# Optimization experiments

Hardware: AMD Instinct MI355X
Metric: run time of the kernel (lower is better)

## Reference

```python
import jax, jax.numpy as jnp
import numpy as np

B, S, D = 4, 2048, 512
H, DK, DV = 8, 64, 64
DFF = 2048
LN_EPS = 1e-5


def _layernorm(x, g, b):
    mu = jnp.mean(x, axis=-1, keepdims=True)
    var = jnp.mean(jnp.square(x - mu), axis=-1, keepdims=True)
    return (x - mu) * jax.lax.rsqrt(var + LN_EPS) * g + b


def setup_inputs() -> dict:
    key = jax.random.key(0)
    ks = jax.random.split(key, 9)
    def xavier(k, shape):
        fan_out, fan_in = shape
        std = np.sqrt(2.0 / (fan_in + fan_out))
        return jax.random.normal(k, shape, jnp.float32) * std
    GELU_GAIN = 1.85
    return {
        "x": jax.random.normal(ks[0], (B, S, D), jnp.float32),
        "attention_mask": jax.random.randint(ks[1], (B, S), 0, 2).astype(bool),
        "Wq": xavier(ks[2], (H * DK, D)),
        "Wk": xavier(ks[3], (H * DK, D)),
        "Wv": xavier(ks[4], (H * DV, D)),
        "Wp": xavier(ks[5], (D, H * DV)),
        "W1": xavier(ks[6], (DFF, D)) * GELU_GAIN,
        "b1": jnp.zeros((DFF,), jnp.float32),
        "W2": xavier(ks[7], (D, DFF)),
        "b2": jnp.zeros((D,), jnp.float32),
        "ln1_g": jnp.ones((D,), jnp.float32),
        "ln1_b": jnp.zeros((D,), jnp.float32),
        "ln2_g": jnp.ones((D,), jnp.float32),
        "ln2_b": jnp.zeros((D,), jnp.float32),
    }


def reference(x, attention_mask, Wq, Wk, Wv, Wp, W1, b1, W2, b2,
              ln1_g, ln1_b, ln2_g, ln2_b):
    b, s, d = x.shape
    residual = x
    q = (x @ Wq.T).reshape(b, s, H, DK)  # [B,S,H,DK]
    k = (x @ Wk.T).reshape(b, s, H, DK)
    v = (x @ Wv.T).reshape(b, s, H, DV)
    score = jnp.einsum("bshd,bthd->bhst", q, k) * (DK ** -0.5)  # [B,H,S,S]
    # subtractive mask: score -= 100 * not(mask)
    score = score - 100.0 * (~attention_mask)[:, None, None, :].astype(score.dtype)
    p = jax.nn.softmax(score, axis=-1)
    ctx = jnp.einsum("bhst,bthd->bshd", p, v).reshape(b, s, H * DV)
    att = ctx @ Wp.T  # dropout p=0.1 is identity in eval
    h = _layernorm(att + residual, ln1_g, ln1_b)
    ff = jax.nn.gelu(h @ W1.T + b1, approximate=False) @ W2.T + b2
    out = _layernorm(ff + h, ln2_g, ln2_b)
    return out
```

## Files before the change

### kernel.cpp

```cpp
#include <hip/hip_runtime.h>
#include <cstdint>
#include <cstddef>

#define B_ 4
#define S_ 2048
#define D_ 512
#define H_ 8
#define DK_ 64
#define DFF_ 2048

using s16x8  = __attribute__((ext_vector_type(8))) short;
using bf16x8 = __attribute__((ext_vector_type(8))) __bf16;
using f32x4  = __attribute__((ext_vector_type(4))) float;

__device__ __forceinline__ short f2bf(float f) {
  unsigned u = __builtin_bit_cast(unsigned, f);
  u += 0x7FFFu + ((u >> 16) & 1u);
  return (short)(u >> 16);
}
__device__ __forceinline__ float bf2f(short s) {
  unsigned u = ((unsigned)(unsigned short)s) << 16;
  return __builtin_bit_cast(float, u);
}

__device__ __forceinline__ void gl2lds16(const void* g, void* l) {
  __builtin_amdgcn_global_load_lds(
      (const __attribute__((address_space(1))) void*)g,
      (__attribute__((address_space(3))) void*)l, 16, 0, 0);
}

__global__ __launch_bounds__(256)
void cvt_all(const float* __restrict__ x, const float* __restrict__ Wq,
             const float* __restrict__ Wk, const float* __restrict__ Wv,
             const float* __restrict__ Wp, const float* __restrict__ W1,
             const float* __restrict__ W2,
             short* __restrict__ xb, short* __restrict__ wqkv,
             short* __restrict__ wp, short* __restrict__ w1, short* __restrict__ w2) {
  int blk = blockIdx.x;
  const float* src; short* dst; int off;
  if (blk < 4096)      { src = x;  dst = xb;            off = blk; }
  else if (blk < 4352) { src = Wq; dst = wqkv;          off = blk - 4096; }
  else if (blk < 4608) { src = Wk; dst = wqkv + 262144; off = blk - 4352; }
  else if (blk < 4864) { src = Wv; dst = wqkv + 524288; off = blk - 4608; }
  else if (blk < 5120) { src = Wp; dst = wp;            off = blk - 4864; }
  else if (blk < 6144) { src = W1; dst = w1;            off = blk - 5120; }
  else                 { src = W2; dst = w2;            off = blk - 6144; }
  int i = (off * 256 + threadIdx.x) * 4;
  float4 v = *(const float4*)(src + i);
  *(short4*)(dst + i) = make_short4(f2bf(v.x), f2bf(v.y), f2bf(v.z), f2bf(v.w));
}

__global__ __launch_bounds__(256)
void mask_all(const void* __restrict__ m, float* __restrict__ mb) {
  __shared__ unsigned red[4];
  const unsigned* mw = (const unsigned*)m;
  const int t = threadIdx.x;
  unsigned v = 0;
#pragma unroll
  for (int i = 0; i < 8; ++i) v |= mw[t + i * 256];
#pragma unroll
  for (int s = 1; s < 64; s <<= 1) v |= __shfl_xor(v, s);
  if ((t & 63) == 0) red[t >> 6] = v;
  __syncthreads();
  unsigned f = red[0] | red[1] | red[2] | red[3];
  int i = blockIdx.x * 256 + t;
  int val;
  if ((f & ~1u) == 0u)            val = ((const int*)m)[i];
  else if (f == 0x3F800000u)      val = (((const float*)m)[i] != 0.0f);
  else                            val = ((const unsigned char*)m)[i];
  mb[i] = val ? 0.0f : -100.0f;
}

template <int MODE>
__global__ __launch_bounds__(256)
void gemm_bt(const short* __restrict__ A, const short* __restrict__ B,
             int M, int N, int K,
             const float* __restrict__ aux1,
             void* __restrict__ out0, void* __restrict__ out1, void* __restrict__ out2) {
  __shared__ alignas(16) short As[128][64];
  __shared__ alignas(16) short Bs[128][64];

  const int tid  = threadIdx.x;
  const int lane = tid & 63;
  const int wave = tid >> 6;
  const int quad = lane >> 4;
  const int l16  = lane & 15;
  const int wm   = (wave >> 1) * 64;
  const int wn   = (wave & 1) * 64;
  const int bm   = blockIdx.x * 128;
  const int bn   = blockIdx.y * 128;
  const int Kh   = K / gridDim.z;
  const int koff = blockIdx.z * Kh;

  const int srow8 = lane >> 3;
  const int pb    = lane & 7;

  f32x4 acc[4][4] = {};

  for (int k0 = 0; k0 < Kh; k0 += 64) {
#pragma unroll
    for (int i = 0; i < 4; ++i) {
      const int rr = wave * 32 + i * 8 + srow8;
      const int cb = pb ^ (rr & 7);
      gl2lds16(A + (size_t)(bm + rr) * K + koff + k0 + cb * 8, &As[wave * 32 + i * 8][0]);
      gl2lds16(B + (size_t)(bn + rr) * K + koff + k0 + cb * 8, &Bs[wave * 32 + i * 8][0]);
    }
    __syncthreads();

#pragma unroll
    for (int c = 0; c < 2; ++c) {
      bf16x8 a[4], b[4];
#pragma unroll
      for (int i = 0; i < 4; ++i) {
        const int row = wm + i * 16 + l16;
        const int pba = (c * 4 + quad) ^ (row & 7);
        a[i] = __builtin_bit_cast(bf16x8, *(const s16x8*)&As[row][pba * 8]);
      }
#pragma unroll
      for (int j = 0; j < 4; ++j) {
        const int row = wn + j * 16 + l16;
        const int pbb = (c * 4 + quad) ^ (row & 7);
        b[j] = __builtin_bit_cast(bf16x8, *(const s16x8*)&Bs[row][pbb * 8]);
      }
#pragma unroll
      for (int i = 0; i < 4; ++i)
#pragma unroll
        for (int j = 0; j < 4; ++j)
          acc[i][j] = __builtin_amdgcn_mfma_f32_16x16x32_bf16(a[i], b[j], acc[i][j], 0, 0, 0);
    }
    __syncthreads();
  }

#pragma unroll
  for (int i = 0; i < 4; ++i) {
    const int m0 = bm + wm + i * 16 + quad * 4;
#pragma unroll
    for (int j = 0; j < 4; ++j) {
      const int n = bn + wn + j * 16 + l16;
      if constexpr (MODE == 0) {
        const int bb = m0 >> 11, ss0 = m0 & 2047;
        if (n < 512) {
          short4 pk = make_short4(f2bf(acc[i][j][0] * 0.125f), f2bf(acc[i][j][1] * 0.125f),
                                  f2bf(acc[i][j][2] * 0.125f), f2bf(acc[i][j][3] * 0.125f));
          *(short4*)((short*)out0 +
              ((((size_t)bb * H_ + (n >> 6)) * 64 + (n & 63)) * S_ + ss0)) = pk;
        } else if (n >= 1024) {
          const int nn = n - 1024;
          short4 pk = make_short4(f2bf(acc[i][j][0]), f2bf(acc[i][j][1]),
                                  f2bf(acc[i][j][2]), f2bf(acc[i][j][3]));
          *(short4*)((short*)out2 +
              ((((size_t)bb * H_ + (nn >> 6)) * 64 + (nn & 63)) * S_ + ss0)) = pk;
        } else {
          const int nn = n - 512;
          const size_t rowb = ((size_t)bb * H_ + (nn >> 6)) * S_ + ss0;
#pragma unroll
          for (int rr = 0; rr < 4; ++rr)
            ((short*)out1)[(rowb + rr) * 64 + (nn & 63)] = f2bf(acc[i][j][rr]);
        }
      } else if constexpr (MODE == 1) {
        float* dst = (float*)out0 + (size_t)blockIdx.z * M * N;
#pragma unroll
        for (int rr = 0; rr < 4; ++rr)
          dst[(size_t)(m0 + rr) * N + n] = acc[i][j][rr];
      } else {
#pragma unroll
        for (int rr = 0; rr < 4; ++rr) {
          float t = acc[i][j][rr] + aux1[n];
          float gl = 0.5f * t * (1.0f + erff(t * 0.70710678118f));
          ((short*)out0)[(size_t)(m0 + rr) * N + n] = f2bf(gl);
        }
      }
    }
  }
}

__global__ __launch_bounds__(256)
void flash_attn_mfma(const short* __restrict__ QTg, const short* __restrict__ Kb,
                     const short* __restrict__ Vtg, const float* __restrict__ maskbias,
                     short* __restrict__ ctxb) {
  __shared__ alignas(16) short Ks[64][72];
  __shared__ alignas(16) short Vt[64][72];
  __shared__ alignas(16) short Ps[4][32][72];
  __shared__ alignas(16) float mrow[S_];

  const int b = blockIdx.z, h = blockIdx.y;
  const int tid = threadIdx.x;
  const int w = tid >> 6, lane = tid & 63;
  const int quad = lane >> 4, l16 = lane & 15;
  const size_t base  = ((size_t)(b * H_ + h)) * S_ * DK_;
  const size_t baseT = ((size_t)(b * H_ + h)) * DK_ * S_;
  const int q0 = blockIdx.x * 128;

  {
    const float4* mp = (const float4*)(maskbias + (size_t)b * S_);
    ((float4*)mrow)[tid]       = mp[tid];
    ((float4*)mrow)[tid + 256] = mp[tid + 256];
  }

  bf16x8 qa[2][2];
#pragma unroll
  for (int st = 0; st < 2; ++st) {
    const int q = q0 + w * 32 + st * 16 + l16;
#pragma unroll
    for (int c = 0; c < 2; ++c) {
      s16x8 t;
#pragma unroll
      for (int j = 0; j < 8; ++j)
        t[j] = QTg[baseT + (size_t)(c * 32 + quad * 8 + j) * S_ + q];
      qa[st][c] = __builtin_bit_cast(bf16x8, t);
    }
  }

  f32x4 Oc[2][4] = {};
  float li[2][4] = {};

  const int r = tid >> 2, c16 = (tid & 3) * 16;
  const short* kp = Kb  + base  + (size_t)r * 64 + c16;
  const short* vp = Vtg + baseT + (size_t)r * S_ + c16;

  s16x8 kr0 = *(const s16x8*)(kp);
  s16x8 kr1 = *(const s16x8*)(kp + 8);
  s16x8 vr0 = *(const s16x8*)(vp);
  s16x8 vr1 = *(const s16x8*)(vp + 8);

  for (int t0 = 0; t0 < S_; t0 += 64) {
    __syncthreads();
    *(s16x8*)&Ks[r][c16]     = kr0;
    *(s16x8*)&Ks[r][c16 + 8] = kr1;
    *(s16x8*)&Vt[r][c16]     = vr0;
    *(s16x8*)&Vt[r][c16 + 8] = vr1;
    __syncthreads();

    if (t0 + 64 < S_) {
      kr0 = *(const s16x8*)(kp + (size_t)(t0 + 64) * 64);
      kr1 = *(const s16x8*)(kp + (size_t)(t0 + 64) * 64 + 8);
      vr0 = *(const s16x8*)(vp + t0 + 64);
      vr1 = *(const s16x8*)(vp + t0 + 64 + 8);
    }

    f32x4 sc[2][4] = {};
#pragma unroll
    for (int c = 0; c < 2; ++c) {
#pragma unroll
      for (int jt = 0; jt < 4; ++jt) {
        bf16x8 kb = __builtin_bit_cast(bf16x8,
            *(const s16x8*)&Ks[jt * 16 + l16][c * 32 + quad * 8]);
        sc[0][jt] = __builtin_amdgcn_mfma_f32_16x16x32_bf16(qa[0][c], kb, sc[0][jt], 0, 0, 0);
        sc[1][jt] = __builtin_amdgcn_mfma_f32_16x16x32_bf16(qa[1][c], kb, sc[1][jt], 0, 0, 0);
      }
    }

    float mb4[4];
#pragma unroll
    for (int jt = 0; jt < 4; ++jt) mb4[jt] = mrow[t0 + jt * 16 + l16];
#pragma unroll
    for (int st = 0; st < 2; ++st) {
#pragma unroll
      for (int jt = 0; jt < 4; ++jt) {
#pragma unroll
        for (int rr = 0; rr < 4; ++rr) {
          float p = __expf(sc[st][jt][rr] + mb4[jt]);
          unsigned u = __builtin_bit_cast(unsigned, p) & 0xFFFF0000u;
          li[st][rr] += __builtin_bit_cast(float, u);
          Ps[w][st * 16 + quad * 4 + rr][jt * 16 + l16] = (short)(u >> 16);
        }
      }
    }

#pragma unroll
    for (int c = 0; c < 2; ++c) {
      bf16x8 pa0 = __builtin_bit_cast(bf16x8,
          *(const s16x8*)&Ps[w][l16][c * 32 + quad * 8]);
      bf16x8 pa1 = __builtin_bit_cast(bf16x8,
          *(const s16x8*)&Ps[w][16 + l16][c * 32 + quad * 8]);
#pragma unroll
      for (int dt = 0; dt < 4; ++dt) {
        bf16x8 vb = __builtin_bit_cast(bf16x8,
            *(const s16x8*)&Vt[dt * 16 + l16][c * 32 + quad * 8]);
        Oc[0][dt] = __builtin_amdgcn_mfma_f32_16x16x32_bf16(pa0, vb, Oc[0][dt], 0, 0, 0);
        Oc[1][dt] = __builtin_amdgcn_mfma_f32_16x16x32_bf16(pa1, vb, Oc[1][dt], 0, 0, 0);
      }
    }
  }

#pragma unroll
  for (int st = 0; st < 2; ++st) {
#pragma unroll
    for (int rr = 0; rr < 4; ++rr) {
      float l = li[st][rr];
#pragma unroll
      for (int m = 1; m < 16; m <<= 1) l += __shfl_xor(l, m);
      float inv = 1.f / l;
      const size_t row = (size_t)b * S_ + q0 + w * 32 + st * 16 + quad * 4 + rr;
#pragma unroll
      for (int dt = 0; dt < 4; ++dt)
        ctxb[row * (H_ * DK_) + h * 64 + dt * 16 + l16] = f2bf(Oc[st][dt][rr] * inv);
    }
  }
}

__global__ __launch_bounds__(256)
void ln_fused(const float* __restrict__ p0, const float* __restrict__ p1,
              const float* __restrict__ xres, const short* __restrict__ hres,
              const float* __restrict__ bias,
              const float* __restrict__ g, const float* __restrict__ bb,
              float* __restrict__ out32, short* __restrict__ outb) {
  const int wave = threadIdx.x >> 6, lane = threadIdx.x & 63;
  const int token = blockIdx.x * 4 + wave;
  const size_t off = (size_t)token * D_;
  const int c = lane * 8;

  float v[8];
  {
    float4 a0 = *(const float4*)(p0 + off + c);
    float4 a1 = *(const float4*)(p0 + off + c + 4);
    float4 b0 = *(const float4*)(p1 + off + c);
    float4 b1 = *(const float4*)(p1 + off + c + 4);
    v[0]=a0.x+b0.x; v[1]=a0.y+b0.y; v[2]=a0.z+b0.z; v[3]=a0.w+b0.w;
    v[4]=a1.x+b1.x; v[5]=a1.y+b1.y; v[6]=a1.z+b1.z; v[7]=a1.w+b1.w;
  }
  if (xres) {
    float4 x0 = *(const float4*)(xres + off + c);
    float4 x1 = *(const float4*)(xres + off + c + 4);
    v[0]+=x0.x; v[1]+=x0.y; v[2]+=x0.z; v[3]+=x0.w;
    v[4]+=x1.x; v[5]+=x1.y; v[6]+=x1.z; v[7]+=x1.w;
  }
  if (hres) {
    short4 h0 = *(const short4*)(hres + off + c);
    short4 h1 = *(const short4*)(hres + off + c + 4);
    v[0]+=bf2f(h0.x); v[1]+=bf2f(h0.y); v[2]+=bf2f(h0.z); v[3]+=bf2f(h0.w);
    v[4]+=bf2f(h1.x); v[5]+=bf2f(h1.y); v[6]+=bf2f(h1.z); v[7]+=bf2f(h1.w);
  }
  if (bias) {
    float4 c0 = *(const float4*)(bias + c);
    float4 c1 = *(const float4*)(bias + c + 4);
    v[0]+=c0.x; v[1]+=c0.y; v[2]+=c0.z; v[3]+=c0.w;
    v[4]+=c1.x; v[5]+=c1.y; v[6]+=c1.z; v[7]+=c1.w;
  }

  float sum = 0.f;
#pragma unroll
  for (int i = 0; i < 8; ++i) sum += v[i];
#pragma unroll
  for (int m = 1; m < 64; m <<= 1) sum += __shfl_xor(sum, m);
  float mu = sum * (1.0f / D_);
  float vs = 0.f;
#pragma unroll
  for (int i = 0; i < 8; ++i) { v[i] -= mu; vs += v[i] * v[i]; }
#pragma unroll
  for (int m = 1; m < 64; m <<= 1) vs += __shfl_xor(vs, m);
  float rstd = rsqrtf(vs * (1.0f / D_) + 1e-5f);
#pragma unroll
  for (int i = 0; i < 8; ++i) {
    float val = v[i] * rstd * g[c + i] + bb[c + i];
    if (out32) out32[off + c + i] = val;
    if (outb)  outb[off + c + i] = f2bf(val);
  }
}

constexpr size_t OFF_XB   = 0;
constexpr size_t OFF_WQKV = 8388608;
constexpr size_t OFF_WP   = 9961472;
constexpr size_t OFF_W1   = 10485760;
constexpr size_t OFF_W2   = 12582912;
constexpr size_t OFF_QT   = 14680064;
constexpr size_t OFF_K    = 23068672;
constexpr size_t OFF_VT   = 31457280;
constexpr size_t OFF_CTX  = 39845888;
constexpr size_t OFF_P0   = 48234496;
constexpr size_t OFF_P1   = 65011712;
constexpr size_t OFF_HB   = 81788928;
constexpr size_t OFF_FF1  = 14680064;
constexpr size_t OFF_MB   = 90177536;
constexpr size_t WS_NEED  = 90210304;

extern "C" void kernel_launch(void* const* d_in, const int* in_sizes, int n_in,
                              void* d_out, int out_size, void* d_ws, size_t ws_size,
                              hipStream_t stream) {
  if (ws_size < WS_NEED) return;

  const float* x    = (const float*)d_in[0];
  const void*  msk  = d_in[1];
  const float* Wq   = (const float*)d_in[2];
  const float* Wk   = (const float*)d_in[3];
  const float* Wv   = (const float*)d_in[4];
  const float* Wp   = (const float*)d_in[5];
  const float* W1   = (const float*)d_in[6];
  const float* b1   = (const float*)d_in[7];
  const float* W2   = (const float*)d_in[8];
  const float* b2   = (const float*)d_in[9];
  const float* ln1g = (const float*)d_in[10];
  const float* ln1b = (const float*)d_in[11];
  const float* ln2g = (const float*)d_in[12];
  const float* ln2b = (const float*)d_in[13];

  char* ws = (char*)d_ws;
  short* xb    = (short*)(ws + OFF_XB);
  short* wqkv  = (short*)(ws + OFF_WQKV);
  short* Wpb   = (short*)(ws + OFF_WP);
  short* W1b   = (short*)(ws + OFF_W1);
  short* W2b   = (short*)(ws + OFF_W2);
  short* QTb   = (short*)(ws + OFF_QT);
  short* Kbh   = (short*)(ws + OFF_K);
  short* VTb   = (short*)(ws + OFF_VT);
  short* ctxb  = (short*)(ws + OFF_CTX);
  float* p0    = (float*)(ws + OFF_P0);
  short* hb    = (short*)(ws + OFF_HB);
  short* ff1b  = (short*)(ws + OFF_FF1);
  float* mbias = (float*)(ws + OFF_MB);

  mask_all<<<32, 256, 0, stream>>>(msk, mbias);

  cvt_all<<<7168, 256, 0, stream>>>(x, Wq, Wk, Wv, Wp, W1, W2,
                                    xb, wqkv, Wpb, W1b, W2b);

  gemm_bt<0><<<dim3(64, 12, 1), 256, 0, stream>>>(xb, wqkv, 8192, 1536, 512,
                                                  nullptr, QTb, Kbh, VTb);

  flash_attn_mfma<<<dim3(S_ / 128, H_, B_), 256, 0, stream>>>(QTb, Kbh, VTb, mbias, ctxb);

  gemm_bt<1><<<dim3(64, 4, 2), 256, 0, stream>>>(ctxb, Wpb, 8192, 512, 512,
                                                 nullptr, p0, nullptr, nullptr);

  ln_fused<<<2048, 256, 0, stream>>>(p0, p0 + (size_t)8192 * 512, x, nullptr, nullptr,
                                     ln1g, ln1b, nullptr, hb);

  gemm_bt<2><<<dim3(64, 16, 1), 256, 0, stream>>>(hb, W1b, 8192, 2048, 512,
                                                  b1, ff1b, nullptr, nullptr);

  gemm_bt<1><<<dim3(64, 4, 2), 256, 0, stream>>>(ff1b, W2b, 8192, 512, 2048,
                                                 nullptr, p0, nullptr, nullptr);

  ln_fused<<<2048, 256, 0, stream>>>(p0, p0 + (size_t)8192 * 512, nullptr, hb, b2,
                                     ln2g, ln2b, (float*)d_out, nullptr);
}
```

Before: 325.0 us.

## Load K/V MFMA fragments directly from global memory, swizzle P tile in LDS

```diff
diff --git a/kernel.cpp b/kernel.cpp
--- a/kernel.cpp
+++ b/kernel.cpp
@@ -174,12 +174,10 @@
   }
 }
 
-__global__ __launch_bounds__(256)
+__global__ __launch_bounds__(256, 2)
 void flash_attn_mfma(const short* __restrict__ QTg, const short* __restrict__ Kb,
                      const short* __restrict__ Vtg, const float* __restrict__ maskbias,
                      short* __restrict__ ctxb) {
-  __shared__ alignas(16) short Ks[64][72];
-  __shared__ alignas(16) short Vt[64][72];
   __shared__ alignas(16) short Ps[4][32][72];
   __shared__ alignas(16) float mrow[S_];
 
@@ -196,6 +194,7 @@
     ((float4*)mrow)[tid]       = mp[tid];
     ((float4*)mrow)[tid + 256] = mp[tid + 256];
   }
+  __syncthreads();
 
   bf16x8 qa[2][2];
 #pragma unroll
@@ -213,38 +212,18 @@
 
   f32x4 Oc[2][4] = {};
   float li[2][4] = {};
-
-  const int r = tid >> 2, c16 = (tid & 3) * 16;
-  const short* kp = Kb  + base  + (size_t)r * 64 + c16;
-  const short* vp = Vtg + baseT + (size_t)r * S_ + c16;
-
-  s16x8 kr0 = *(const s16x8*)(kp);
-  s16x8 kr1 = *(const s16x8*)(kp + 8);
-  s16x8 vr0 = *(const s16x8*)(vp);
-  s16x8 vr1 = *(const s16x8*)(vp + 8);
+  const int swz = l16 & 7;
+  const short* kfrag = Kb  + base  + quad * 8;
+  const short* vfrag = Vtg + baseT + quad * 8;
 
   for (int t0 = 0; t0 < S_; t0 += 64) {
-    __syncthreads();
-    *(s16x8*)&Ks[r][c16]     = kr0;
-    *(s16x8*)&Ks[r][c16 + 8] = kr1;
-    *(s16x8*)&Vt[r][c16]     = vr0;
-    *(s16x8*)&Vt[r][c16 + 8] = vr1;
-    __syncthreads();
-
-    if (t0 + 64 < S_) {
-      kr0 = *(const s16x8*)(kp + (size_t)(t0 + 64) * 64);
-      kr1 = *(const s16x8*)(kp + (size_t)(t0 + 64) * 64 + 8);
-      vr0 = *(const s16x8*)(vp + t0 + 64);
-      vr1 = *(const s16x8*)(vp + t0 + 64 + 8);
-    }
-
     f32x4 sc[2][4] = {};
 #pragma unroll
     for (int c = 0; c < 2; ++c) {
 #pragma unroll
       for (int jt = 0; jt < 4; ++jt) {
         bf16x8 kb = __builtin_bit_cast(bf16x8,
-            *(const s16x8*)&Ks[jt * 16 + l16][c * 32 + quad * 8]);
+            *(const s16x8*)(kfrag + (size_t)(t0 + jt * 16 + l16) * 64 + c * 32));
         sc[0][jt] = __builtin_amdgcn_mfma_f32_16x16x32_bf16(qa[0][c], kb, sc[0][jt], 0, 0, 0);
         sc[1][jt] = __builtin_amdgcn_mfma_f32_16x16x32_bf16(qa[1][c], kb, sc[1][jt], 0, 0, 0);
       }
@@ -262,7 +241,9 @@
           float p = __expf(sc[st][jt][rr] + mb4[jt]);
           unsigned u = __builtin_bit_cast(unsigned, p) & 0xFFFF0000u;
           li[st][rr] += __builtin_bit_cast(float, u);
-          Ps[w][st * 16 + quad * 4 + rr][jt * 16 + l16] = (short)(u >> 16);
+          const int row = st * 16 + quad * 4 + rr;
+          const int blk = (jt * 2 + (l16 >> 3)) ^ (row & 7);
+          Ps[w][row][blk * 8 + (l16 & 7)] = (short)(u >> 16);
         }
       }
     }
@@ -270,13 +251,13 @@
 #pragma unroll
     for (int c = 0; c < 2; ++c) {
       bf16x8 pa0 = __builtin_bit_cast(bf16x8,
-          *(const s16x8*)&Ps[w][l16][c * 32 + quad * 8]);
+          *(const s16x8*)&Ps[w][l16][(((c * 4 + quad) ^ swz)) * 8]);
       bf16x8 pa1 = __builtin_bit_cast(bf16x8,
-          *(const s16x8*)&Ps[w][16 + l16][c * 32 + quad * 8]);
+          *(const s16x8*)&Ps[w][16 + l16][(((c * 4 + quad) ^ swz)) * 8]);
 #pragma unroll
       for (int dt = 0; dt < 4; ++dt) {
         bf16x8 vb = __builtin_bit_cast(bf16x8,
-            *(const s16x8*)&Vt[dt * 16 + l16][c * 32 + quad * 8]);
+            *(const s16x8*)(vfrag + (size_t)(dt * 16 + l16) * S_ + t0 + c * 32));
         Oc[0][dt] = __builtin_amdgcn_mfma_f32_16x16x32_bf16(pa0, vb, Oc[0][dt], 0, 0, 0);
         Oc[1][dt] = __builtin_amdgcn_mfma_f32_16x16x32_bf16(pa1, vb, Oc[1][dt], 0, 0, 0);
       }
```

Measured after the change: 405.0 us. 24.6% more time.

## Fuse mask preprocessing into attention kernel and swizzle P tile in LDS

Applied to the files above, without the earlier changes.

```diff
diff --git a/kernel.cpp b/kernel.cpp
--- a/kernel.cpp
+++ b/kernel.cpp
@@ -50,27 +50,6 @@
   *(short4*)(dst + i) = make_short4(f2bf(v.x), f2bf(v.y), f2bf(v.z), f2bf(v.w));
 }
 
-__global__ __launch_bounds__(256)
-void mask_all(const void* __restrict__ m, float* __restrict__ mb) {
-  __shared__ unsigned red[4];
-  const unsigned* mw = (const unsigned*)m;
-  const int t = threadIdx.x;
-  unsigned v = 0;
-#pragma unroll
-  for (int i = 0; i < 8; ++i) v |= mw[t + i * 256];
-#pragma unroll
-  for (int s = 1; s < 64; s <<= 1) v |= __shfl_xor(v, s);
-  if ((t & 63) == 0) red[t >> 6] = v;
-  __syncthreads();
-  unsigned f = red[0] | red[1] | red[2] | red[3];
-  int i = blockIdx.x * 256 + t;
-  int val;
-  if ((f & ~1u) == 0u)            val = ((const int*)m)[i];
-  else if (f == 0x3F800000u)      val = (((const float*)m)[i] != 0.0f);
-  else                            val = ((const unsigned char*)m)[i];
-  mb[i] = val ? 0.0f : -100.0f;
-}
-
 template <int MODE>
 __global__ __launch_bounds__(256)
 void gemm_bt(const short* __restrict__ A, const short* __restrict__ B,
@@ -176,12 +155,13 @@
 
 __global__ __launch_bounds__(256)
 void flash_attn_mfma(const short* __restrict__ QTg, const short* __restrict__ Kb,
-                     const short* __restrict__ Vtg, const float* __restrict__ maskbias,
+                     const short* __restrict__ Vtg, const void* __restrict__ mraw,
                      short* __restrict__ ctxb) {
   __shared__ alignas(16) short Ks[64][72];
   __shared__ alignas(16) short Vt[64][72];
-  __shared__ alignas(16) short Ps[4][32][72];
+  __shared__ alignas(16) short Ps[4][32][64];
   __shared__ alignas(16) float mrow[S_];
+  __shared__ unsigned red[4];
 
   const int b = blockIdx.z, h = blockIdx.y;
   const int tid = threadIdx.x;
@@ -192,9 +172,25 @@
   const int q0 = blockIdx.x * 128;
 
   {
-    const float4* mp = (const float4*)(maskbias + (size_t)b * S_);
-    ((float4*)mrow)[tid]       = mp[tid];
-    ((float4*)mrow)[tid + 256] = mp[tid + 256];
+    const unsigned* mw = (const unsigned*)mraw;
+    unsigned v = 0;
+#pragma unroll
+    for (int i = 0; i < 8; ++i) v |= mw[tid + i * 256];
+#pragma unroll
+    for (int s = 1; s < 64; s <<= 1) v |= __shfl_xor(v, s);
+    if (lane == 0) red[w] = v;
+    __syncthreads();
+    unsigned f = red[0] | red[1] | red[2] | red[3];
+#pragma unroll
+    for (int i = 0; i < 8; ++i) {
+      int idx = tid + i * 256;
+      int gidx = b * S_ + idx;
+      int val;
+      if ((f & ~1u) == 0u)            val = ((const int*)mraw)[gidx];
+      else if (f == 0x3F800000u)      val = (((const float*)mraw)[gidx] != 0.0f);
+      else                            val = ((const unsigned char*)mraw)[gidx];
+      mrow[idx] = val ? 0.0f : -100.0f;
+    }
   }
 
   bf16x8 qa[2][2];
@@ -213,6 +209,7 @@
 
   f32x4 Oc[2][4] = {};
   float li[2][4] = {};
+  const int swz = l16 & 7;
 
   const int r = tid >> 2, c16 = (tid & 3) * 16;
   const short* kp = Kb  + base  + (size_t)r * 64 + c16;
@@ -262,7 +259,9 @@
           float p = __expf(sc[st][jt][rr] + mb4[jt]);
           unsigned u = __builtin_bit_cast(unsigned, p) & 0xFFFF0000u;
           li[st][rr] += __builtin_bit_cast(float, u);
-          Ps[w][st * 16 + quad * 4 + rr][jt * 16 + l16] = (short)(u >> 16);
+          const int row = st * 16 + quad * 4 + rr;
+          const int blk = (jt * 2 + (l16 >> 3)) ^ (row & 7);
+          Ps[w][row][blk * 8 + (l16 & 7)] = (short)(u >> 16);
         }
       }
     }
@@ -270,9 +269,9 @@
 #pragma unroll
     for (int c = 0; c < 2; ++c) {
       bf16x8 pa0 = __builtin_bit_cast(bf16x8,
-          *(const s16x8*)&Ps[w][l16][c * 32 + quad * 8]);
+          *(const s16x8*)&Ps[w][l16][((c * 4 + quad) ^ swz) * 8]);
       bf16x8 pa1 = __builtin_bit_cast(bf16x8,
-          *(const s16x8*)&Ps[w][16 + l16][c * 32 + quad * 8]);
+          *(const s16x8*)&Ps[w][16 + l16][((c * 4 + quad) ^ swz) * 8]);
 #pragma unroll
       for (int dt = 0; dt < 4; ++dt) {
         bf16x8 vb = __builtin_bit_cast(bf16x8,
@@ -371,8 +370,7 @@
 constexpr size_t OFF_P1   = 65011712;
 constexpr size_t OFF_HB   = 81788928;
 constexpr size_t OFF_FF1  = 14680064;
-constexpr size_t OFF_MB   = 90177536;
-constexpr size_t WS_NEED  = 90210304;
+constexpr size_t WS_NEED  = 90177536;
 
 extern "C" void kernel_launch(void* const* d_in, const int* in_sizes, int n_in,
                               void* d_out, int out_size, void* d_ws, size_t ws_size,
@@ -407,9 +405,6 @@
   float* p0    = (float*)(ws + OFF_P0);
   short* hb    = (short*)(ws + OFF_HB);
   short* ff1b  = (short*)(ws + OFF_FF1);
-  float* mbias = (float*)(ws + OFF_MB);
-
-  mask_all<<<32, 256, 0, stream>>>(msk, mbias);
 
   cvt_all<<<7168, 256, 0, stream>>>(x, Wq, Wk, Wv, Wp, W1, W2,
                                     xb, wqkv, Wpb, W1b, W2b);
@@ -417,7 +412,7 @@
   gemm_bt<0><<<dim3(64, 12, 1), 256, 0, stream>>>(xb, wqkv, 8192, 1536, 512,
                                                   nullptr, QTb, Kbh, VTb);
 
-  flash_attn_mfma<<<dim3(S_ / 128, H_, B_), 256, 0, stream>>>(QTb, Kbh, VTb, mbias, ctxb);
+  flash_attn_mfma<<<dim3(S_ / 128, H_, B_), 256, 0, stream>>>(QTb, Kbh, VTb, msk, ctxb);
 
   gemm_bt<1><<<dim3(64, 4, 2), 256, 0, stream>>>(ctxb, Wpb, 8192, 512, 512,
                                                  nullptr, p0, nullptr, nullptr);
```

Result: faster. 314.7 us (-3.2%).
